# Performance work log

Measured on AMD Instinct MI355X. Metric: run time of the kernel, lower is better.

Reference implementation:

```python
import jax, jax.numpy as jnp
import numpy as np

EMBED = 128
HEADS = 32          # embed_dim // 4, forced by fuse Conv2d channel counts
HEAD_DIM = EMBED // HEADS  # 4
WS = (4, 7, 7)
N = WS[0] * WS[1] * WS[2]  # 196 tokens per window
B = 64              # batch * num_windows
SCALE = HEAD_DIM ** -0.5
EPS = 1e-5


def _rel_index():
    d, h, w = WS
    coords = np.stack(np.meshgrid(np.arange(d), np.arange(h), np.arange(w), indexing='ij'))
    flat = coords.reshape(3, -1)                       # [3, N]
    rel = (flat[:, :, None] - flat[:, None, :]).transpose(1, 2, 0).astype(np.int64)  # [N,N,3]
    rel[:, :, 0] += d - 1
    rel[:, :, 1] += h - 1
    rel[:, :, 2] += w - 1
    rel[:, :, 0] *= (2 * h - 1) * (2 * w - 1)
    rel[:, :, 1] *= (2 * w - 1)
    return rel.sum(-1).astype(np.int32)                # [N, N]


def setup_inputs() -> dict:
    key = jax.random.key(0)
    ks = jax.random.split(key, 7)
    d, h, w = WS
    tbl = (2 * d - 1) * (2 * h - 1) * (2 * w - 1)
    return {
        'x_in':      jax.random.normal(ks[0], (B, N, EMBED), dtype=jnp.float32),
        'x_in2':     jax.random.normal(ks[1], (B, N, EMBED), dtype=jnp.float32),
        'qkv_w':     jax.random.normal(ks[2], (3 * EMBED, EMBED), dtype=jnp.float32) * 0.02,
        'proj_w':    jax.random.normal(ks[3], (EMBED, EMBED), dtype=jnp.float32) * 0.02,
        'proj_b':    jnp.zeros((EMBED,), dtype=jnp.float32),
        'rpb_table': jax.random.normal(ks[4], (tbl, HEADS), dtype=jnp.float32) * 0.02,
        'fuse_w':    jax.random.normal(ks[5], (EMBED // 4, EMBED // 2), dtype=jnp.float32) * 0.1,
        'fuse_b':    jnp.zeros((EMBED // 4,), dtype=jnp.float32),
        'rel_idx':   jnp.asarray(_rel_index()),
    }


def _branch(x, qkv_w):
    b, n, c = x.shape
    qkv = (x @ qkv_w.T).reshape(b, n, 3, HEADS, c // HEADS).transpose(2, 0, 3, 1, 4)
    q, k, v = qkv[0] * SCALE, qkv[1], qkv[2]           # [b, H, n, d]
    attn = jnp.einsum('bhnd,bhmd->bhnm', q, k)         # [b, H, n, n]
    return attn, v


def reference(x_in, x_in2, qkv_w, proj_w, proj_b, rpb_table, fuse_w, fuse_b, rel_idx):
    b, n, c = x_in.shape
    attn1, v1 = _branch(x_in, qkv_w)
    attn2, v2 = _branch(x_in2, qkv_w)

    # conv-gated value fusion: Conv2d 1x1 over channel dim (= 2H) + InstanceNorm2d + ReLU + Sigmoid
    vcat = jnp.concatenate([v1, v2], axis=1)           # [b, 2H, n, d]
    v = jnp.einsum('bcnd,oc->bond', vcat, fuse_w) + fuse_b[None, :, None, None]  # [b, H, n, d]
    mu = v.mean(axis=(2, 3), keepdims=True)
    var = v.var(axis=(2, 3), keepdims=True)            # biased, as InstanceNorm2d
    v = (v - mu) * jax.lax.rsqrt(var + EPS)
    v = jax.nn.sigmoid(jax.nn.relu(v))

    # relative position bias: gather [n*n] rows of table -> [H, n, n]
    bias = rpb_table[rel_idx[:n, :n].reshape(-1)].reshape(n, n, HEADS).transpose(2, 0, 1)

    attn = jax.nn.softmax(attn1 + attn2 + bias[None], axis=-1)  # [b, H, n, n]
    x = jnp.einsum('bhnm,bhmd->bhnd', attn, v).transpose(0, 2, 1, 3).reshape(b, n, c)
    return x @ proj_w.T + proj_b
```

## Files before the change

kernel.cpp:

```cpp
#include <hip/hip_runtime.h>
#include <hip/hip_bf16.h>
#include <stdint.h>

#define NB   64
#define NTOK 196
#define NH   32
#define HD   4
#define CE   128
#define NM   38416

typedef __bf16 bf16x8 __attribute__((ext_vector_type(8)));
typedef short  bf16x4s __attribute__((ext_vector_type(4)));
typedef float  f32x4  __attribute__((ext_vector_type(4)));

#define QSCALE 0.7213475204444817f
#define LOG2E  1.4426950408889634f

__device__ __forceinline__ float u2f(unsigned short u) {
    union { unsigned int i; float f; } z;
    z.i = ((unsigned int)u) << 16;
    return z.f;
}
__device__ __forceinline__ unsigned short f2u(float f) {
    union { float f; unsigned int i; } z; z.f = f;
    unsigned int x = z.i;
    return (unsigned short)((x + 0x7fffu + ((x >> 16) & 1u)) >> 16);
}

extern "C" __global__ __launch_bounds__(256) void qkv_bias(
    const float* __restrict__ x1,
    const float* __restrict__ x2,
    const float* __restrict__ qkvw,
    const int* __restrict__ rel_idx, const float* __restrict__ rpb,
    unsigned short* __restrict__ Qb, unsigned short* __restrict__ Kb,
    unsigned short* __restrict__ V, unsigned short* __restrict__ biasM)
{
    __shared__ alignas(16) unsigned short AT[64][136];
    __shared__ alignas(16) unsigned short BT[64][136];
    const int tid = threadIdx.x;

    if (blockIdx.y == 6) {
        const int bx = blockIdx.x;
        const int qt = bx % 13, h = bx / 13;
        const int lane = tid & 63, wv = tid >> 6;
        const int quad = lane >> 4, tc = lane & 15;
        for (int nt = wv; nt < 14; nt += 4) {
            union { uint2 v; unsigned short s[4]; } e;
#pragma unroll
            for (int r = 0; r < 4; ++r) {
                int q   = qt * 16 + tc;
                int key = nt * 16 + quad * 4 + r;
                unsigned short u = 0xFF80;
                if (q < 196 && key < 196) {
                    int idx = rel_idx[q * 196 + key];
                    u = f2u(rpb[idx * 32 + h] * LOG2E);
                }
                e.s[r] = u;
            }
            unsigned int off = (((h * 13 + qt) * 7 + (nt >> 1)) * 64 + lane) * 8
                               + (nt & 1) * 4;
            *(uint2*)(biasM + off) = e.v;
        }
        return;
    }
    if (blockIdx.x >= 392) return;

    const int r0 = blockIdx.x * 64;
    const int j0 = blockIdx.y * 64;

    for (int idx = tid; idx < 2048; idx += 256) {
        int row = idx >> 5, k0 = (idx & 31) << 2;
        int r = r0 + row;
        const float* xp = (r >= 12544) ? x2 : x1;
        int rem = r - ((r >= 12544) ? 12544 : 0);
        float4 v = *(const float4*)&xp[rem * 128 + k0];
        ushort4 u; u.x = f2u(v.x); u.y = f2u(v.y); u.z = f2u(v.z); u.w = f2u(v.w);
        *(ushort4*)&AT[row][k0] = u;
    }
    for (int idx = tid; idx < 2048; idx += 256) {
        int row = idx >> 5, k0 = (idx & 31) << 2;
        float4 v = *(const float4*)&qkvw[(j0 + row) * 128 + k0];
        ushort4 u; u.x = f2u(v.x); u.y = f2u(v.y); u.z = f2u(v.z); u.w = f2u(v.w);
        *(ushort4*)&BT[row][k0] = u;
    }
    __syncthreads();

    const int lane = tid & 63, w = tid >> 6;
    const int wj = (w >> 1) * 32;
    const int wt = (w & 1) * 32;
    const int quad = lane >> 4, tc = lane & 15;

    f32x4 acc[2][2] = {};
#pragma unroll
    for (int ks = 0; ks < 4; ++ks) {
        int k0 = ks * 32 + quad * 8;
        bf16x8 a0 = *(const bf16x8*)&BT[wj + tc][k0];
        bf16x8 a1 = *(const bf16x8*)&BT[wj + 16 + tc][k0];
        bf16x8 b0 = *(const bf16x8*)&AT[wt + tc][k0];
        bf16x8 b1 = *(const bf16x8*)&AT[wt + 16 + tc][k0];
        acc[0][0] = __builtin_amdgcn_mfma_f32_16x16x32_bf16(a0, b0, acc[0][0], 0, 0, 0);
        acc[0][1] = __builtin_amdgcn_mfma_f32_16x16x32_bf16(a0, b1, acc[0][1], 0, 0, 0);
        acc[1][0] = __builtin_amdgcn_mfma_f32_16x16x32_bf16(a1, b0, acc[1][0], 0, 0, 0);
        acc[1][1] = __builtin_amdgcn_mfma_f32_16x16x32_bf16(a1, b1, acc[1][1], 0, 0, 0);
    }

    const int sel = j0 >> 7;
#pragma unroll
    for (int mi = 0; mi < 2; ++mi) {
        int jbase = (j0 + wj + mi * 16 + quad * 4) & 127;
        int hh = jbase >> 2;
#pragma unroll
        for (int ni = 0; ni < 2; ++ni) {
            int tok = r0 + wt + ni * 16 + tc;
            int branch = (tok >= 12544) ? 1 : 0;
            int rem = tok - branch * 12544;
            int bb = rem / 196;
            int nn = rem - bb * 196;
            union { uint2 v; unsigned short s[4]; } pk2;
            if (sel == 0) {
#pragma unroll
                for (int r = 0; r < 4; ++r) pk2.s[r] = f2u(acc[mi][ni][r] * QSCALE);
                *(uint2*)&Qb[((bb * 32 + hh) * 196 + nn) * 8 + branch * 4] = pk2.v;
            } else if (sel == 1) {
#pragma unroll
                for (int r = 0; r < 4; ++r) pk2.s[r] = f2u(acc[mi][ni][r]);
                *(uint2*)&Kb[((bb * 32 + hh) * 196 + nn) * 8 + branch * 4] = pk2.v;
            } else {
#pragma unroll
                for (int r = 0; r < 4; ++r) pk2.s[r] = f2u(acc[mi][ni][r]);
                *(uint2*)&V[(bb * 64 + branch * 32 + hh) * 784 + nn * 4] = pk2.v;
            }
        }
    }
}

__device__ __forceinline__ float block_sum(float v, float* red, int tid) {
#pragma unroll
    for (int off = 32; off > 0; off >>= 1) v += __shfl_down(v, off);
    __syncthreads();
    if ((tid & 63) == 0) red[tid >> 6] = v;
    __syncthreads();
    return red[0] + red[1] + red[2] + red[3];
}

__device__ __forceinline__ float act_sig_relu(float x) {
    return x > 0.f ? __fdividef(1.f, 1.f + __expf(-x)) : 0.5f;
}

extern "C" __global__ __launch_bounds__(256) void fuse_kernel(
    const unsigned short* __restrict__ V,
    const float* __restrict__ fuse_w,
    const float* __restrict__ fuse_b,
    unsigned short* __restrict__ VfT)
{
    const int b = blockIdx.x, o0 = blockIdx.y * 4;
    const int tid = threadIdx.x;
    __shared__ float fws[4][64];
    __shared__ float red[4];
    fws[tid >> 6][tid & 63] = fuse_w[(o0 + (tid >> 6)) * 64 + (tid & 63)];
    __syncthreads();

    const bool act = tid < 196;
    const unsigned short* Vb = V + b * 64 * 784 + tid * 4;
    float4 a[4] = {};
    for (int c = 0; c < 64; ++c) {
        float4 x = {0.f, 0.f, 0.f, 0.f};
        if (act) {
            uint2 u = *(const uint2*)(Vb + c * 784);
            union { unsigned int i; float f; } z;
            z.i = u.x << 16;          x.x = z.f;
            z.i = u.x & 0xffff0000u;  x.y = z.f;
            z.i = u.y << 16;          x.z = z.f;
            z.i = u.y & 0xffff0000u;  x.w = z.f;
        }
#pragma unroll
        for (int o = 0; o < 4; ++o) {
            float w0 = fws[o][c];
            a[o].x = fmaf(w0, x.x, a[o].x);
            a[o].y = fmaf(w0, x.y, a[o].y);
            a[o].z = fmaf(w0, x.z, a[o].z);
            a[o].w = fmaf(w0, x.w, a[o].w);
        }
    }

    const float inv784 = 1.0f / 784.0f;
#pragma unroll
    for (int o = 0; o < 4; ++o) {
        float fb0 = fuse_b[o0 + o];
        float4 v = a[o];
        if (act) { v.x += fb0; v.y += fb0; v.z += fb0; v.w += fb0; }
        float s = v.x + v.y + v.z + v.w;
        float q = v.x*v.x + v.y*v.y + v.z*v.z + v.w*v.w;
        float S = block_sum(s, red, tid);
        float Q = block_sum(q, red, tid);
        float mu = S * inv784;
        float rstd = rsqrtf(Q * inv784 - mu * mu + 1e-5f);
        if (act) {
            unsigned short* op = VfT + (unsigned)(b * 32 + o0 + o) * 784 + tid;
            op[0 * 196] = f2u(act_sig_relu((v.x - mu) * rstd));
            op[1 * 196] = f2u(act_sig_relu((v.y - mu) * rstd));
            op[2 * 196] = f2u(act_sig_relu((v.z - mu) * rstd));
            op[3 * 196] = f2u(act_sig_relu((v.w - mu) * rstd));
        }
    }
}

extern "C" __global__ __launch_bounds__(256) void attn_kernel(
    const unsigned short* __restrict__ Qb, const unsigned short* __restrict__ Kb,
    const unsigned short* __restrict__ VfT, const unsigned short* __restrict__ biasM,
    unsigned short* __restrict__ Ob)
{
    const int bh = blockIdx.x;
    const int b = bh >> 5, h = bh & 31;
    __shared__ alignas(16) unsigned short Qs[208][8];
    __shared__ alignas(16) unsigned short Ks[224][8];
    __shared__ alignas(16) unsigned short VT[16][232];
    const int tid = threadIdx.x;

    const unsigned short* Qrow = Qb + bh * 1568;
    const unsigned short* Krow = Kb + bh * 1568;
    if (tid < 208) {
        uint4 z = {0, 0, 0, 0};
        uint4 v = (tid < 196) ? *(const uint4*)(Qrow + tid * 8) : z;
        *(uint4*)&Qs[tid][0] = v;
    }
    if (tid < 224) {
        uint4 z = {0, 0, 0, 0};
        uint4 v = (tid < 196) ? *(const uint4*)(Krow + tid * 8) : z;
        *(uint4*)&Ks[tid][0] = v;
    }
    {
        unsigned int* vtw = (unsigned int*)&VT[0][0];
        for (int i = tid; i < 580; i += 256) vtw[i] = 0u;
    }
    __syncthreads();
    if (tid < 196) {
        uint2 u = ((const uint2*)(VfT + (unsigned)bh * 784))[tid];
        int d = tid / 49;
        int n = (tid - d * 49) * 4;
        *(uint2*)&VT[d][n] = u;
    }
    if (tid < 98) *(unsigned int*)&VT[4][tid * 2] = 0x3F803F80u;
    __syncthreads();

    const int lane = tid & 63, wv = tid >> 6;
    const int quad = lane >> 4, tc = lane & 15;

    bf16x8 bq[4];
#pragma unroll
    for (int i = 0; i < 4; ++i) {
        int qt = wv + 4 * i;
        int qtc = qt > 12 ? 12 : qt;
        bf16x8 z = {};
        bq[i] = z;
        if (quad == 0) bq[i] = *(const bf16x8*)&Qs[qtc * 16 + tc][0];
    }

    const unsigned short* bias_h = biasM + (unsigned)(h * 13) * 3584;
    f32x4 O[4] = {};

#pragma unroll 2
    for (int kt = 0; kt < 7; ++kt) {
        bf16x8 ka0 = *(const bf16x8*)&Ks[(kt * 2 + 0) * 16 + tc][0];
        bf16x8 ka1 = *(const bf16x8*)&Ks[(kt * 2 + 1) * 16 + tc][0];
        bf16x4s vf0 = *(const bf16x4s*)&VT[tc][(kt * 2 + 0) * 16 + quad * 4];
        bf16x4s vf1 = *(const bf16x4s*)&VT[tc][(kt * 2 + 1) * 16 + quad * 4];
#pragma unroll
        for (int i = 0; i < 4; ++i) {
            int qt = wv + 4 * i;
            int qtc = qt > 12 ? 12 : qt;
            uint4 bw = *(const uint4*)(bias_h + qtc * 3584 + kt * 512 + lane * 8);
            f32x4 s0, s1;
            {
                union { unsigned int u; float f; } c;
                c.u = bw.x << 16;          s0[0] = c.f;
                c.u = bw.x & 0xffff0000u;  s0[1] = c.f;
                c.u = bw.y << 16;          s0[2] = c.f;
                c.u = bw.y & 0xffff0000u;  s0[3] = c.f;
                c.u = bw.z << 16;          s1[0] = c.f;
                c.u = bw.z & 0xffff0000u;  s1[1] = c.f;
                c.u = bw.w << 16;          s1[2] = c.f;
                c.u = bw.w & 0xffff0000u;  s1[3] = c.f;
            }
            s0 = __builtin_amdgcn_mfma_f32_16x16x32_bf16(ka0, bq[i], s0, 0, 0, 0);
            s1 = __builtin_amdgcn_mfma_f32_16x16x32_bf16(ka1, bq[i], s1, 0, 0, 0);
            float e0 = __builtin_amdgcn_exp2f(s0[0]);
            float e1 = __builtin_amdgcn_exp2f(s0[1]);
            float e2 = __builtin_amdgcn_exp2f(s0[2]);
            float e3 = __builtin_amdgcn_exp2f(s0[3]);
            float g0 = __builtin_amdgcn_exp2f(s1[0]);
            float g1 = __builtin_amdgcn_exp2f(s1[1]);
            float g2 = __builtin_amdgcn_exp2f(s1[2]);
            float g3 = __builtin_amdgcn_exp2f(s1[3]);
            union { int d[2]; bf16x4s v; } pf0, pf1;
            pf0.d[0] = (int)__builtin_amdgcn_perm(__float_as_uint(e1), __float_as_uint(e0), 0x07060302u);
            pf0.d[1] = (int)__builtin_amdgcn_perm(__float_as_uint(e3), __float_as_uint(e2), 0x07060302u);
            pf1.d[0] = (int)__builtin_amdgcn_perm(__float_as_uint(g1), __float_as_uint(g0), 0x07060302u);
            pf1.d[1] = (int)__builtin_amdgcn_perm(__float_as_uint(g3), __float_as_uint(g2), 0x07060302u);
            O[i] = __builtin_amdgcn_mfma_f32_16x16x16bf16_1k(vf0, pf0.v, O[i], 0, 0, 0);
            O[i] = __builtin_amdgcn_mfma_f32_16x16x16bf16_1k(vf1, pf1.v, O[i], 0, 0, 0);
        }
    }

#pragma unroll
    for (int i = 0; i < 4; ++i) {
        float rs = __shfl(O[i][0], 16 + tc);
        int q = (wv + 4 * i) * 16 + tc;
        if (quad == 0 && q < 196) {
            float inv = __builtin_amdgcn_rcpf(rs);
            union { uint2 v; unsigned short s[4]; } pk2;
            pk2.s[0] = f2u(O[i][0] * inv);
            pk2.s[1] = f2u(O[i][1] * inv);
            pk2.s[2] = f2u(O[i][2] * inv);
            pk2.s[3] = f2u(O[i][3] * inv);
            *(uint2*)&Ob[(b * 196 + q) * 128 + h * 4] = pk2.v;
        }
    }
}

extern "C" __global__ __launch_bounds__(256) void proj_kernel(
    const unsigned short* __restrict__ Ob, const float* __restrict__ projw,
    const float* __restrict__ projb, float* __restrict__ out)
{
    __shared__ alignas(16) unsigned short AT[64][136];
    __shared__ alignas(16) unsigned short BT[64][136];
    const int tid = threadIdx.x;
    const int r0 = blockIdx.x * 64;
    const int j0 = blockIdx.y * 64;

    for (int idx = tid; idx < 1024; idx += 256) {
        int row = idx >> 4, k0 = (idx & 15) << 3;
        *(uint4*)&AT[row][k0] = *(const uint4*)&Ob[(r0 + row) * 128 + k0];
    }
    for (int idx = tid; idx < 2048; idx += 256) {
        int row = idx >> 5, k0 = (idx & 31) << 2;
        float4 v = *(const float4*)&projw[(j0 + row) * 128 + k0];
        ushort4 u; u.x = f2u(v.x); u.y = f2u(v.y); u.z = f2u(v.z); u.w = f2u(v.w);
        *(ushort4*)&BT[row][k0] = u;
    }
    __syncthreads();

    const int lane = tid & 63, w = tid >> 6;
    const int wm = (w >> 1) * 32, wn = (w & 1) * 32;
    const int quad = lane >> 4, tcol = lane & 15;

    f32x4 acc[2][2] = {};
#pragma unroll
    for (int ks = 0; ks < 4; ++ks) {
        int k0 = ks * 32 + quad * 8;
        bf16x8 a0 = *(const bf16x8*)&AT[wm + tcol][k0];
        bf16x8 a1 = *(const bf16x8*)&AT[wm + 16 + tcol][k0];
        bf16x8 b0 = *(const bf16x8*)&BT[wn + tcol][k0];
        bf16x8 b1 = *(const bf16x8*)&BT[wn + 16 + tcol][k0];
        acc[0][0] = __builtin_amdgcn_mfma_f32_16x16x32_bf16(a0, b0, acc[0][0], 0, 0, 0);
        acc[0][1] = __builtin_amdgcn_mfma_f32_16x16x32_bf16(a0, b1, acc[0][1], 0, 0, 0);
        acc[1][0] = __builtin_amdgcn_mfma_f32_16x16x32_bf16(a1, b0, acc[1][0], 0, 0, 0);
        acc[1][1] = __builtin_amdgcn_mfma_f32_16x16x32_bf16(a1, b1, acc[1][1], 0, 0, 0);
    }

#pragma unroll
    for (int mi = 0; mi < 2; ++mi) {
#pragma unroll
        for (int ni = 0; ni < 2; ++ni) {
            int j = j0 + wn + ni * 16 + tcol;
            float pb = projb[j];
#pragma unroll
            for (int reg = 0; reg < 4; ++reg) {
                int r = r0 + wm + mi * 16 + quad * 4 + reg;
                out[r * 128 + j] = acc[mi][ni][reg] + pb;
            }
        }
    }
}

extern "C" void kernel_launch(void* const* d_in, const int* in_sizes, int n_in,
                              void* d_out, int out_size, void* d_ws, size_t ws_size,
                              hipStream_t stream)
{
    const float* x1    = (const float*)d_in[0];
    const float* x2    = (const float*)d_in[1];
    const float* qkvw  = (const float*)d_in[2];
    const float* projw = (const float*)d_in[3];
    const float* projb = (const float*)d_in[4];
    const float* rpb   = (const float*)d_in[5];
    const float* fw    = (const float*)d_in[6];
    const float* fb    = (const float*)d_in[7];
    const int*   rel   = (const int*)d_in[8];
    float* out = (float*)d_out;

    char* w = (char*)d_ws;
    unsigned short* Qb  = (unsigned short*)(w);
    unsigned short* Kb  = (unsigned short*)(w + 6422528);
    unsigned short* V   = (unsigned short*)(w + 12845056);
    unsigned short* VfT = (unsigned short*)(w + 19267584);
    unsigned short* bM  = (unsigned short*)(w + 22478848);
    unsigned short* Ob  = (unsigned short*)(w + 25460736);

    qkv_bias  <<<dim3(416, 7), dim3(256), 0, stream>>>(x1, x2, qkvw, rel, rpb,
                                                       Qb, Kb, V, bM);
    fuse_kernel<<<dim3(64, 8),  dim3(256), 0, stream>>>(V, fw, fb, VfT);
    attn_kernel<<<dim3(2048),   dim3(256), 0, stream>>>(Qb, Kb, VfT, bM, Ob);
    proj_kernel<<<dim3(196, 2), dim3(256), 0, stream>>>(Ob, projw, projb, out);
}
```

Before: 156.0 us.

## Widen QKV tiles, batch InstanceNorm reductions, read Q/K directly in attention

The QKV GEMM now gives each block 128 output columns instead of 64, so the launch shrinks from 7 to 4 column groups (one of them still builds the bias table) and each input row is loaded and converted to bf16 fewer times. The fuse kernel merges its eight separate block reductions into one pass with a single barrier. The attention kernel drops LDS staging of Q and K and loads MFMA fragments straight from global memory. The direct K/Q loads now read unpadded neighbouring rows for tokens past 196, relying on the -inf bias to mask them. The larger QKV tile also uses more LDS and registers per block.

```diff
diff --git a/kernel.cpp b/kernel.cpp
--- a/kernel.cpp
+++ b/kernel.cpp
@@ -36,10 +36,10 @@
     unsigned short* __restrict__ V, unsigned short* __restrict__ biasM)
 {
     __shared__ alignas(16) unsigned short AT[64][136];
-    __shared__ alignas(16) unsigned short BT[64][136];
+    __shared__ alignas(16) unsigned short BT[128][136];
     const int tid = threadIdx.x;
 
-    if (blockIdx.y == 6) {
+    if (blockIdx.y == 3) {
         const int bx = blockIdx.x;
         const int qt = bx % 13, h = bx / 13;
         const int lane = tid & 63, wv = tid >> 6;
@@ -66,7 +66,8 @@
     if (blockIdx.x >= 392) return;
 
     const int r0 = blockIdx.x * 64;
-    const int j0 = blockIdx.y * 64;
+    const int sel = blockIdx.y;
+    const int j0 = sel * 128;
 
     for (int idx = tid; idx < 2048; idx += 256) {
         int row = idx >> 5, k0 = (idx & 31) << 2;
@@ -77,7 +78,7 @@
         ushort4 u; u.x = f2u(v.x); u.y = f2u(v.y); u.z = f2u(v.z); u.w = f2u(v.w);
         *(ushort4*)&AT[row][k0] = u;
     }
-    for (int idx = tid; idx < 2048; idx += 256) {
+    for (int idx = tid; idx < 4096; idx += 256) {
         int row = idx >> 5, k0 = (idx & 31) << 2;
         float4 v = *(const float4*)&qkvw[(j0 + row) * 128 + k0];
         ushort4 u; u.x = f2u(v.x); u.y = f2u(v.y); u.z = f2u(v.z); u.w = f2u(v.w);
@@ -86,32 +87,30 @@
     __syncthreads();
 
     const int lane = tid & 63, w = tid >> 6;
-    const int wj = (w >> 1) * 32;
-    const int wt = (w & 1) * 32;
+    const int wj = w * 32;
     const int quad = lane >> 4, tc = lane & 15;
 
-    f32x4 acc[2][2] = {};
+    f32x4 acc[2][4] = {};
 #pragma unroll
     for (int ks = 0; ks < 4; ++ks) {
         int k0 = ks * 32 + quad * 8;
         bf16x8 a0 = *(const bf16x8*)&BT[wj + tc][k0];
         bf16x8 a1 = *(const bf16x8*)&BT[wj + 16 + tc][k0];
-        bf16x8 b0 = *(const bf16x8*)&AT[wt + tc][k0];
-        bf16x8 b1 = *(const bf16x8*)&AT[wt + 16 + tc][k0];
-        acc[0][0] = __builtin_amdgcn_mfma_f32_16x16x32_bf16(a0, b0, acc[0][0], 0, 0, 0);
-        acc[0][1] = __builtin_amdgcn_mfma_f32_16x16x32_bf16(a0, b1, acc[0][1], 0, 0, 0);
-        acc[1][0] = __builtin_amdgcn_mfma_f32_16x16x32_bf16(a1, b0, acc[1][0], 0, 0, 0);
-        acc[1][1] = __builtin_amdgcn_mfma_f32_16x16x32_bf16(a1, b1, acc[1][1], 0, 0, 0);
-    }
-
-    const int sel = j0 >> 7;
+#pragma unroll
+        for (int ni = 0; ni < 4; ++ni) {
+            bf16x8 b = *(const bf16x8*)&AT[ni * 16 + tc][k0];
+            acc[0][ni] = __builtin_amdgcn_mfma_f32_16x16x32_bf16(a0, b, acc[0][ni], 0, 0, 0);
+            acc[1][ni] = __builtin_amdgcn_mfma_f32_16x16x32_bf16(a1, b, acc[1][ni], 0, 0, 0);
+        }
+    }
+
 #pragma unroll
     for (int mi = 0; mi < 2; ++mi) {
-        int jbase = (j0 + wj + mi * 16 + quad * 4) & 127;
-        int hh = jbase >> 2;
-#pragma unroll
-        for (int ni = 0; ni < 2; ++ni) {
-            int tok = r0 + wt + ni * 16 + tc;
+        int jl = wj + mi * 16 + quad * 4;
+        int hh = jl >> 2;
+#pragma unroll
+        for (int ni = 0; ni < 4; ++ni) {
+            int tok = r0 + ni * 16 + tc;
             int branch = (tok >= 12544) ? 1 : 0;
             int rem = tok - branch * 12544;
             int bb = rem / 196;
@@ -132,15 +131,6 @@
             }
         }
     }
-}
-
-__device__ __forceinline__ float block_sum(float v, float* red, int tid) {
-#pragma unroll
-    for (int off = 32; off > 0; off >>= 1) v += __shfl_down(v, off);
-    __syncthreads();
-    if ((tid & 63) == 0) red[tid >> 6] = v;
-    __syncthreads();
-    return red[0] + red[1] + red[2] + red[3];
 }
 
 __device__ __forceinline__ float act_sig_relu(float x) {
@@ -156,7 +146,7 @@
     const int b = blockIdx.x, o0 = blockIdx.y * 4;
     const int tid = threadIdx.x;
     __shared__ float fws[4][64];
-    __shared__ float red[4];
+    __shared__ float redS[4][4], redQ[4][4];
     fws[tid >> 6][tid & 63] = fuse_w[(o0 + (tid >> 6)) * 64 + (tid & 63)];
     __syncthreads();
 
@@ -183,19 +173,44 @@
         }
     }
 
+    float sv[4], qv[4];
+#pragma unroll
+    for (int o = 0; o < 4; ++o) {
+        float4 v = a[o];
+        if (act) {
+            float fb0 = fuse_b[o0 + o];
+            v.x += fb0; v.y += fb0; v.z += fb0; v.w += fb0;
+        }
+        a[o] = v;
+        sv[o] = v.x + v.y + v.z + v.w;
+        qv[o] = v.x*v.x + v.y*v.y + v.z*v.z + v.w*v.w;
+    }
+#pragma unroll
+    for (int off = 32; off > 0; off >>= 1) {
+#pragma unroll
+        for (int o = 0; o < 4; ++o) {
+            sv[o] += __shfl_down(sv[o], off);
+            qv[o] += __shfl_down(qv[o], off);
+        }
+    }
+    if ((tid & 63) == 0) {
+#pragma unroll
+        for (int o = 0; o < 4; ++o) {
+            redS[tid >> 6][o] = sv[o];
+            redQ[tid >> 6][o] = qv[o];
+        }
+    }
+    __syncthreads();
+
     const float inv784 = 1.0f / 784.0f;
-#pragma unroll
-    for (int o = 0; o < 4; ++o) {
-        float fb0 = fuse_b[o0 + o];
-        float4 v = a[o];
-        if (act) { v.x += fb0; v.y += fb0; v.z += fb0; v.w += fb0; }
-        float s = v.x + v.y + v.z + v.w;
-        float q = v.x*v.x + v.y*v.y + v.z*v.z + v.w*v.w;
-        float S = block_sum(s, red, tid);
-        float Q = block_sum(q, red, tid);
-        float mu = S * inv784;
-        float rstd = rsqrtf(Q * inv784 - mu * mu + 1e-5f);
-        if (act) {
+    if (act) {
+#pragma unroll
+        for (int o = 0; o < 4; ++o) {
+            float S = redS[0][o] + redS[1][o] + redS[2][o] + redS[3][o];
+            float Q = redQ[0][o] + redQ[1][o] + redQ[2][o] + redQ[3][o];
+            float mu = S * inv784;
+            float rstd = rsqrtf(Q * inv784 - mu * mu + 1e-5f);
+            float4 v = a[o];
             unsigned short* op = VfT + (unsigned)(b * 32 + o0 + o) * 784 + tid;
             op[0 * 196] = f2u(act_sig_relu((v.x - mu) * rstd));
             op[1 * 196] = f2u(act_sig_relu((v.y - mu) * rstd));
@@ -212,23 +227,11 @@
 {
     const int bh = blockIdx.x;
     const int b = bh >> 5, h = bh & 31;
-    __shared__ alignas(16) unsigned short Qs[208][8];
-    __shared__ alignas(16) unsigned short Ks[224][8];
     __shared__ alignas(16) unsigned short VT[16][232];
     const int tid = threadIdx.x;
-
-    const unsigned short* Qrow = Qb + bh * 1568;
-    const unsigned short* Krow = Kb + bh * 1568;
-    if (tid < 208) {
-        uint4 z = {0, 0, 0, 0};
-        uint4 v = (tid < 196) ? *(const uint4*)(Qrow + tid * 8) : z;
-        *(uint4*)&Qs[tid][0] = v;
-    }
-    if (tid < 224) {
-        uint4 z = {0, 0, 0, 0};
-        uint4 v = (tid < 196) ? *(const uint4*)(Krow + tid * 8) : z;
-        *(uint4*)&Ks[tid][0] = v;
-    }
+    const int lane = tid & 63, wv = tid >> 6;
+    const int quad = lane >> 4, tc = lane & 15;
+
     {
         unsigned int* vtw = (unsigned int*)&VT[0][0];
         for (int i = tid; i < 580; i += 256) vtw[i] = 0u;
@@ -243,8 +246,8 @@
     if (tid < 98) *(unsigned int*)&VT[4][tid * 2] = 0x3F803F80u;
     __syncthreads();
 
-    const int lane = tid & 63, wv = tid >> 6;
-    const int quad = lane >> 4, tc = lane & 15;
+    const unsigned short* Qrow = Qb + bh * 1568;
+    const unsigned short* Krow = Kb + bh * 1568;
 
     bf16x8 bq[4];
 #pragma unroll
@@ -253,7 +256,7 @@
         int qtc = qt > 12 ? 12 : qt;
         bf16x8 z = {};
         bq[i] = z;
-        if (quad == 0) bq[i] = *(const bf16x8*)&Qs[qtc * 16 + tc][0];
+        if (quad == 0) bq[i] = *(const bf16x8*)(Qrow + (qtc * 16 + tc) * 8);
     }
 
     const unsigned short* bias_h = biasM + (unsigned)(h * 13) * 3584;
@@ -261,8 +264,8 @@
 
 #pragma unroll 2
     for (int kt = 0; kt < 7; ++kt) {
-        bf16x8 ka0 = *(const bf16x8*)&Ks[(kt * 2 + 0) * 16 + tc][0];
-        bf16x8 ka1 = *(const bf16x8*)&Ks[(kt * 2 + 1) * 16 + tc][0];
+        bf16x8 ka0 = *(const bf16x8*)(Krow + ((kt * 2 + 0) * 16 + tc) * 8);
+        bf16x8 ka1 = *(const bf16x8*)(Krow + ((kt * 2 + 1) * 16 + tc) * 8);
         bf16x4s vf0 = *(const bf16x4s*)&VT[tc][(kt * 2 + 0) * 16 + quad * 4];
         bf16x4s vf1 = *(const bf16x4s*)&VT[tc][(kt * 2 + 1) * 16 + quad * 4];
 #pragma unroll
@@ -396,7 +399,7 @@
     unsigned short* bM  = (unsigned short*)(w + 22478848);
     unsigned short* Ob  = (unsigned short*)(w + 25460736);
 
-    qkv_bias  <<<dim3(416, 7), dim3(256), 0, stream>>>(x1, x2, qkvw, rel, rpb,
+    qkv_bias  <<<dim3(416, 4), dim3(256), 0, stream>>>(x1, x2, qkvw, rel, rpb,
                                                        Qb, Kb, V, bM);
     fuse_kernel<<<dim3(64, 8),  dim3(256), 0, stream>>>(V, fw, fb, VfT);
     attn_kernel<<<dim3(2048),   dim3(256), 0, stream>>>(Qb, Kb, VfT, bM, Ob);
```

Result: no change. 156.5 us (+0.3%).
